# Kernel optimization log

Hardware: AMD Instinct MI355X
Metric: run time of the kernel (lower is better)

The kernel has to match this reference:

```python
import jax, jax.numpy as jnp
import numpy as np

D_MODEL = 1024
N_HEADS = 16
D_KEYS = D_MODEL // N_HEADS


def setup_inputs() -> dict:
    key = jax.random.key(0)
    ks = jax.random.split(key, 11)
    B, L, S = 2, 2048, 2048
    inp = {
        "queries": jax.random.normal(ks[0], (B, L, D_MODEL), dtype=jnp.float32),
        "keys": jax.random.normal(ks[1], (B, S, D_MODEL), dtype=jnp.float32),
        "values": jax.random.normal(ks[2], (B, S, D_MODEL), dtype=jnp.float32),
        # Linear params, scaled like torch default init (~U(-1/sqrt(D), 1/sqrt(D)))
        "Wq": jax.random.normal(ks[3], (D_MODEL, D_MODEL), dtype=jnp.float32) / np.sqrt(D_MODEL),
        "bq": jax.random.normal(ks[4], (D_MODEL,), dtype=jnp.float32) / np.sqrt(D_MODEL),
        "Wk": jax.random.normal(ks[5], (D_MODEL, D_MODEL), dtype=jnp.float32) / np.sqrt(D_MODEL),
        "bk": jax.random.normal(ks[6], (D_MODEL,), dtype=jnp.float32) / np.sqrt(D_MODEL),
        "Wv": jax.random.normal(ks[7], (D_MODEL, D_MODEL), dtype=jnp.float32) / np.sqrt(D_MODEL),
        "bv": jax.random.normal(ks[8], (D_MODEL,), dtype=jnp.float32) / np.sqrt(D_MODEL),
        "Wo": jax.random.normal(ks[9], (D_MODEL, D_MODEL), dtype=jnp.float32) / np.sqrt(D_MODEL),
        "bo": jax.random.normal(ks[10], (D_MODEL,), dtype=jnp.float32) / np.sqrt(D_MODEL),
    }
    return inp


def reference(queries, keys, values, Wq, bq, Wk, bk, Wv, bv, Wo, bo):
    B, L, _ = queries.shape
    S = keys.shape[1]
    H, E = N_HEADS, D_KEYS
    scale = E ** (-0.5)
    q = (queries @ Wq.T + bq).reshape(B, L, H, E)
    k = (keys @ Wk.T + bk).reshape(B, S, H, E)
    v = (values @ Wv.T + bv).reshape(B, S, H, E)
    scores = jnp.einsum('blhe,bshe->bhls', q, k)
    attn = jax.nn.softmax(scores * scale, axis=-1)  # dropout = identity in eval
    out = jnp.einsum('bhls,bshe->blhe', attn, v).reshape(B, L, H * E)
    return out @ Wo.T + bo
```

## Files before the change

kernel.cpp:

```cpp
#include <hip/hip_runtime.h>

typedef unsigned short u16;
typedef unsigned int u32;
typedef __attribute__((ext_vector_type(8))) short short8;
typedef __attribute__((ext_vector_type(4))) short s16x4;
typedef __attribute__((ext_vector_type(4))) float f32x4;
typedef __attribute__((ext_vector_type(16))) float f32x16;

#define DEVI __device__ __forceinline__

#define LSEQ 2048
#define DMODEL 1024
#define NH 16
#define EHD 64

#define QSCALE 0.18033688011112042f

#if __has_builtin(__builtin_amdgcn_exp2f)
#define EXP2(x) __builtin_amdgcn_exp2f(x)
#else
#define EXP2(x) exp2f(x)
#endif

DEVI u16 f2b(float f) {
    u32 u = __float_as_uint(f);
    return (u16)((u + 0x7FFFu + ((u >> 16) & 1u)) >> 16);
}

DEVI u32 cvtpk(float lo, float hi) {
    u32 r;
    asm("v_cvt_pk_bf16_f32 %0, %1, %2" : "=v"(r) : "v"(lo), "v"(hi));
    return r;
}

DEVI void swap32(u32& a, u32& b) {
    asm("v_permlane32_swap_b32 %0, %1" : "+v"(a), "+v"(b));
}

DEVI short8 mk8(u32 a0, u32 a1, u32 a2, u32 a3) {
    union { u32 u[4]; short8 s; } x;
    x.u[0] = a0; x.u[1] = a1; x.u[2] = a2; x.u[3] = a3;
    return x.s;
}

DEVI void async_cp16(const u16* g, u16* l) {
    __builtin_amdgcn_global_load_lds((const __attribute__((address_space(1))) u32*)g,
                                     (__attribute__((address_space(3))) u32*)l, 16, 0, 0);
}

DEVI short8 lds_swz(const u16* base, int row, int colb) {
    int off = (row << 7) + (colb ^ ((row & 7) << 4));
    return *(const short8*)((const char*)base + off);
}

__global__ __launch_bounds__(256) void cvt_all(const float* __restrict__ q,
                                               const float* __restrict__ k,
                                               const float* __restrict__ v,
                                               const float* __restrict__ wq,
                                               const float* __restrict__ wk,
                                               const float* __restrict__ wv,
                                               const float* __restrict__ wo,
                                               u16* __restrict__ dst) {
    const size_t NX8 = (size_t)2 * LSEQ * DMODEL / 8;
    const size_t NW8 = (size_t)DMODEL * DMODEL / 8;
    int bid = blockIdx.x;
    const float* src;
    size_t base;
    int rel;
    if (bid < 2048)      { src = q;  base = 0;             rel = bid; }
    else if (bid < 4096) { src = k;  base = NX8;           rel = bid - 2048; }
    else if (bid < 6144) { src = v;  base = 2 * NX8;       rel = bid - 4096; }
    else if (bid < 6656) { src = wq; base = 3 * NX8;             rel = bid - 6144; }
    else if (bid < 7168) { src = wk; base = 3 * NX8 + NW8;       rel = bid - 6656; }
    else if (bid < 7680) { src = wv; base = 3 * NX8 + 2 * NW8;   rel = bid - 7168; }
    else                 { src = wo; base = 3 * NX8 + 3 * NW8;   rel = bid - 7680; }
    size_t i = (size_t)rel * 256 + threadIdx.x;
    const float4* p = (const float4*)(src + i * 8);
    float4 a = p[0], c = p[1];
    short8 o;
    o[0] = (short)f2b(a.x); o[1] = (short)f2b(a.y);
    o[2] = (short)f2b(a.z); o[3] = (short)f2b(a.w);
    o[4] = (short)f2b(c.x); o[5] = (short)f2b(c.y);
    o[6] = (short)f2b(c.z); o[7] = (short)f2b(c.w);
    *(short8*)(dst + (base + i) * 8) = o;
}

__global__ __launch_bounds__(256) void gemm_qkv(const u16* __restrict__ X,
                                                const u16* __restrict__ W3,
                                                const float* __restrict__ bq,
                                                const float* __restrict__ bk,
                                                const float* __restrict__ bv,
                                                u16* __restrict__ Qp,
                                                u16* __restrict__ Kp,
                                                u16* __restrict__ Vt) {
    __shared__ __align__(16) u16 As[3][4096];
    __shared__ __align__(16) u16 Bs[3][4096];
    const int tid = threadIdx.x;
    const int lane = tid & 63, w = tid >> 6;
    const int lr = lane & 15, lk = lane >> 4;
    const int wr = w >> 1, wc = w & 1;
    const int bid = blockIdx.x;
    const int xcd = bid & 7, rr = bid >> 3;
    const int rb = (xcd * 4 + rr / 24) * 128;
    const int xtile = rr % 24;
    const int cb = xtile * 128;
    const int K = DMODEL;
    const int seg = xtile >> 3;
    const u16* A = X + (size_t)seg * ((size_t)2 * LSEQ * DMODEL);

    f32x4 acc[4][4] = {};

    const int arow = lane >> 2;
    const int acol = (lane & 3) * 8;

#define QKV_STAGE(bb, kk)                                                           \
    do {                                                                            \
        _Pragma("unroll") for (int c2 = 0; c2 < 2; ++c2) {                          \
            int c = w * 2 + c2;                                                     \
            async_cp16(A + (size_t)(rb + c * 16 + arow) * K + (kk) + acol,          \
                       &As[bb][c * 512]);                                           \
            async_cp16(W3 + (size_t)(cb + c * 16 + arow) * K + (kk) + acol,         \
                       &Bs[bb][c * 512]);                                           \
        }                                                                           \
    } while (0)

#define QKV_ITER(bc, bs, tt)                                                          \
    do {                                                                              \
        if ((tt) + 2 < 32) QKV_STAGE(bs, ((tt) + 2) * 32);                            \
        short8 af[4], bfr[4];                                                         \
        _Pragma("unroll") for (int m = 0; m < 4; m++)                                 \
            af[m] = *(const short8*)(&As[bc][(wr * 64 + m * 16 + lr) * 32 + lk * 8]); \
        _Pragma("unroll") for (int n = 0; n < 4; n++)                                 \
            bfr[n] = *(const short8*)(&Bs[bc][(wc * 64 + n * 16 + lr) * 32 + lk * 8]); \
        __builtin_amdgcn_s_setprio(1);                                                \
        _Pragma("unroll") for (int m = 0; m < 4; m++)                                 \
            _Pragma("unroll") for (int n = 0; n < 4; n++)                             \
                acc[m][n] =                                                           \
                    __builtin_amdgcn_mfma_f32_16x16x32_bf16(af[m], bfr[n], acc[m][n], 0, 0, 0); \
        __builtin_amdgcn_s_setprio(0);                                                \
        if ((tt) + 2 < 32) asm volatile("s_waitcnt vmcnt(4)" ::: "memory");           \
        else               asm volatile("s_waitcnt vmcnt(0)" ::: "memory");           \
        __builtin_amdgcn_s_barrier();                                                 \
    } while (0)

    QKV_STAGE(0, 0);
    QKV_STAGE(1, 32);
    asm volatile("s_waitcnt vmcnt(4)" ::: "memory");
    __builtin_amdgcn_s_barrier();

    for (int tb = 0; tb < 30; tb += 3) {
        QKV_ITER(0, 2, tb);
        QKV_ITER(1, 0, tb + 1);
        QKV_ITER(2, 1, tb + 2);
    }
    QKV_ITER(0, 2, 30);
    QKV_ITER(1, 0, 31);

    const float* bp = seg == 0 ? bq : (seg == 1 ? bk : bv);
    const float sc = seg == 0 ? QSCALE : 1.0f;

#pragma unroll
    for (int n = 0; n < 4; n++) {
        int col = cb + wc * 64 + n * 16 + lr;
        int c2 = col & 1023;
        float bvv = bp[c2];
#pragma unroll
        for (int m = 0; m < 4; m++) {
            int row0 = rb + wr * 64 + m * 16 + lk * 4;
            if (seg == 2) {
                s16x4 pk4;
#pragma unroll
                for (int r = 0; r < 4; r++) pk4[r] = (short)f2b(acc[m][n][r] + bvv);
                size_t idx = (((size_t)(row0 >> 11) * NH + (c2 >> 6)) * EHD + (c2 & 63)) * LSEQ +
                             (row0 & (LSEQ - 1));
                *(s16x4*)(Vt + idx) = pk4;
            } else {
                u16* dst = seg == 0 ? Qp : Kp;
#pragma unroll
                for (int r = 0; r < 4; r++)
                    dst[(size_t)(row0 + r) * DMODEL + c2] = f2b((acc[m][n][r] + bvv) * sc);
            }
        }
    }
}

__global__ __launch_bounds__(256) void gemm_out(const u16* __restrict__ A,
                                                const u16* __restrict__ B,
                                                const float* __restrict__ bias,
                                                float* __restrict__ C) {
    __shared__ __align__(16) u16 As[3][4096];
    __shared__ __align__(16) u16 Bs[3][2048];
    const int tid = threadIdx.x;
    const int lane = tid & 63, w = tid >> 6;
    const int lr = lane & 15, lk = lane >> 4;
    const int wr = w >> 1, wc = w & 1;
    const int bid = blockIdx.x;
    const int xcd = bid & 7, rr = bid >> 3;
    const int rb = (xcd * 4 + rr / 16) * 128;
    const int cb = (rr % 16) * 64;
    const int K = DMODEL, N = DMODEL;

    f32x4 acc[4][2] = {};

    const int arow = lane >> 2;
    const int acol = (lane & 3) * 8;

#define OUT_STAGE(bb, kk)                                                           \
    do {                                                                            \
        _Pragma("unroll") for (int c2 = 0; c2 < 2; ++c2) {                          \
            int c = w * 2 + c2;                                                     \
            async_cp16(A + (size_t)(rb + c * 16 + arow) * K + (kk) + acol,          \
                       &As[bb][c * 512]);                                           \
        }                                                                           \
        async_cp16(B + (size_t)(cb + w * 16 + arow) * K + (kk) + acol,              \
                   &Bs[bb][w * 512]);                                               \
    } while (0)

#define OUT_ITER(bc, bs, tt)                                                          \
    do {                                                                              \
        if ((tt) + 2 < 32) OUT_STAGE(bs, ((tt) + 2) * 32);                            \
        short8 af[4], bfr[2];                                                         \
        _Pragma("unroll") for (int m = 0; m < 4; m++)                                 \
            af[m] = *(const short8*)(&As[bc][(wr * 64 + m * 16 + lr) * 32 + lk * 8]); \
        _Pragma("unroll") for (int n = 0; n < 2; n++)                                 \
            bfr[n] = *(const short8*)(&Bs[bc][(wc * 32 + n * 16 + lr) * 32 + lk * 8]); \
        __builtin_amdgcn_s_setprio(1);                                                \
        _Pragma("unroll") for (int m = 0; m < 4; m++)                                 \
            _Pragma("unroll") for (int n = 0; n < 2; n++)                             \
                acc[m][n] =                                                           \
                    __builtin_amdgcn_mfma_f32_16x16x32_bf16(af[m], bfr[n], acc[m][n], 0, 0, 0); \
        __builtin_amdgcn_s_setprio(0);                                                \
        if ((tt) + 2 < 32) asm volatile("s_waitcnt vmcnt(3)" ::: "memory");           \
        else               asm volatile("s_waitcnt vmcnt(0)" ::: "memory");           \
        __builtin_amdgcn_s_barrier();                                                 \
    } while (0)

    OUT_STAGE(0, 0);
    OUT_STAGE(1, 32);
    asm volatile("s_waitcnt vmcnt(3)" ::: "memory");
    __builtin_amdgcn_s_barrier();

    for (int tb = 0; tb < 30; tb += 3) {
        OUT_ITER(0, 2, tb);
        OUT_ITER(1, 0, tb + 1);
        OUT_ITER(2, 1, tb + 2);
    }
    OUT_ITER(0, 2, 30);
    OUT_ITER(1, 0, 31);

#pragma unroll
    for (int n = 0; n < 2; n++) {
        int col = cb + wc * 32 + n * 16 + lr;
        float bv = bias[col];
#pragma unroll
        for (int m = 0; m < 4; m++) {
            int row0 = rb + wr * 64 + m * 16 + lk * 4;
#pragma unroll
            for (int r = 0; r < 4; r++)
                C[(size_t)(row0 + r) * N + col] = acc[m][n][r] + bv;
        }
    }
}

__global__ __launch_bounds__(256) void attn_kernel(const u16* __restrict__ Q,
                                                   const u16* __restrict__ Kp,
                                                   const u16* __restrict__ Vtb,
                                                   u16* __restrict__ Hid) {
    const int bid = blockIdx.x;
    const int j = bid >> 3;
    const int bh = (bid & 7) + 8 * (j >> 4);
    const int q0 = (j & 15) * 128;
    const int b = bh >> 4, h = bh & 15;
    const int tid = threadIdx.x, lane = tid & 63, w = tid >> 6;
    const int l31 = lane & 31, hi = lane >> 5;
    const int qb = q0 + w * 32;

    __shared__ __align__(16) u16 Ks[2][4096];
    __shared__ __align__(16) u16 Vs[2][4096];

    short8 qf[4];
#pragma unroll
    for (int eg = 0; eg < 4; eg++)
        qf[eg] = *(const short8*)(Q + (size_t)(b * LSEQ + qb + l31) * DMODEL + h * EHD +
                                  eg * 16 + hi * 8);

    const int colb = (((lane & 7) ^ (lane >> 3)) << 4);
    size_t kbase[2], vbase[2];
#pragma unroll
    for (int jj = 0; jj < 2; jj++) {
        int row = (jj * 4 + w) * 8 + (lane >> 3);
        kbase[jj] = (size_t)(b * LSEQ + row) * DMODEL + h * EHD + (colb >> 1);
        vbase[jj] = ((size_t)bh * EHD + row) * LSEQ + (colb >> 1);
    }

#define ATTN_STAGE(bb, s0v)                                                           \
    do {                                                                              \
        async_cp16(Kp + kbase[0] + (size_t)(s0v)*DMODEL, &Ks[bb][(0 * 4 + w) * 512]); \
        async_cp16(Kp + kbase[1] + (size_t)(s0v)*DMODEL, &Ks[bb][(1 * 4 + w) * 512]); \
        async_cp16(Vtb + vbase[0] + (s0v), &Vs[bb][(0 * 4 + w) * 512]);               \
        async_cp16(Vtb + vbase[1] + (s0v), &Vs[bb][(1 * 4 + w) * 512]);               \
    } while (0)

    f32x16 o0 = (f32x16)0.f, o1 = (f32x16)0.f, lsum = (f32x16)0.f;
    const u32 one2 = 0x3F803F80u;
    const short8 ones = mk8(one2, one2, one2, one2);

    ATTN_STAGE(0, 0);
    asm volatile("s_waitcnt vmcnt(0)" ::: "memory");
    __syncthreads();

    int cur = 0;
    for (int t = 0; t < LSEQ / 64; ++t) {
        if (t + 1 < LSEQ / 64) ATTN_STAGE(cur ^ 1, (t + 1) * 64);

        f32x16 s0 = (f32x16)0.f, s1 = (f32x16)0.f;
        __builtin_amdgcn_s_setprio(1);
#pragma unroll
        for (int eg = 0; eg < 4; eg++) {
            short8 kf0 = lds_swz(&Ks[cur][0], l31, eg * 32 + hi * 16);
            short8 kf1 = lds_swz(&Ks[cur][0], 32 + l31, eg * 32 + hi * 16);
            s0 = __builtin_amdgcn_mfma_f32_32x32x16_bf16(kf0, qf[eg], s0, 0, 0, 0);
            s1 = __builtin_amdgcn_mfma_f32_32x32x16_bf16(kf1, qf[eg], s1, 0, 0, 0);
        }
        __builtin_amdgcn_s_setprio(0);

#pragma unroll
        for (int r = 0; r < 16; r++) {
            s0[r] = EXP2(s0[r]);
            s1[r] = EXP2(s1[r]);
        }

        short8 paf[4];
#pragma unroll
        for (int kc = 0; kc < 4; kc++) {
            int ro = (kc & 1) * 8;
            u32 u0, u1, u2, u3;
            if (kc < 2) {
                u0 = cvtpk(s0[ro + 0], s0[ro + 1]); u1 = cvtpk(s0[ro + 2], s0[ro + 3]);
                u2 = cvtpk(s0[ro + 4], s0[ro + 5]); u3 = cvtpk(s0[ro + 6], s0[ro + 7]);
            } else {
                u0 = cvtpk(s1[ro + 0], s1[ro + 1]); u1 = cvtpk(s1[ro + 2], s1[ro + 3]);
                u2 = cvtpk(s1[ro + 4], s1[ro + 5]); u3 = cvtpk(s1[ro + 6], s1[ro + 7]);
            }
            swap32(u0, u2);
            swap32(u1, u3);
            paf[kc] = mk8(u0, u1, u2, u3);
        }

        __builtin_amdgcn_s_setprio(1);
#pragma unroll
        for (int kc = 0; kc < 4; kc++) {
            short8 vf0 = lds_swz(&Vs[cur][0], l31, kc * 32 + hi * 16);
            short8 vf1 = lds_swz(&Vs[cur][0], 32 + l31, kc * 32 + hi * 16);
            o0 = __builtin_amdgcn_mfma_f32_32x32x16_bf16(paf[kc], vf0, o0, 0, 0, 0);
            o1 = __builtin_amdgcn_mfma_f32_32x32x16_bf16(paf[kc], vf1, o1, 0, 0, 0);
            lsum = __builtin_amdgcn_mfma_f32_32x32x16_bf16(paf[kc], ones, lsum, 0, 0, 0);
        }
        __builtin_amdgcn_s_setprio(0);

        asm volatile("s_waitcnt vmcnt(0)" ::: "memory");
        __syncthreads();
        cur ^= 1;
    }

#pragma unroll
    for (int r = 0; r < 16; r++) {
        float li = 1.0f / lsum[r];
        int qrow = qb + (r & 3) + 8 * (r >> 2) + 4 * hi;
        size_t base = (size_t)(b * LSEQ + qrow) * DMODEL + h * EHD;
        Hid[base + l31] = f2b(o0[r] * li);
        Hid[base + 32 + l31] = f2b(o1[r] * li);
    }
}

extern "C" void kernel_launch(void* const* d_in, const int* in_sizes, int n_in,
                              void* d_out, int out_size, void* d_ws, size_t ws_size,
                              hipStream_t stream) {
    const float* queries = (const float*)d_in[0];
    const float* keys    = (const float*)d_in[1];
    const float* values  = (const float*)d_in[2];
    const float* Wq = (const float*)d_in[3];
    const float* bq = (const float*)d_in[4];
    const float* Wk = (const float*)d_in[5];
    const float* bk = (const float*)d_in[6];
    const float* Wv = (const float*)d_in[7];
    const float* bv = (const float*)d_in[8];
    const float* Wo = (const float*)d_in[9];
    const float* bo = (const float*)d_in[10];
    float* out = (float*)d_out;

    const size_t NX = (size_t)2 * LSEQ * DMODEL;
    const size_t NW = (size_t)DMODEL * DMODEL;

    u16* p = (u16*)d_ws;
    u16* Xq = p;  p += NX;
    u16* Xk = p;  p += NX;
    u16* Xv = p;  p += NX;
    u16* Wqb = p; p += NW;
    u16* Wkb = p; p += NW;
    u16* Wvb = p; p += NW;
    u16* Wob = p; p += NW;
    u16* Qp = p;  p += NX;
    u16* Kp = p;  p += NX;
    u16* Vt = p;  p += NX;
    u16* Hid = p; p += NX;
    (void)Xk; (void)Xv; (void)Wkb; (void)Wvb;

    cvt_all<<<8192, 256, 0, stream>>>(queries, keys, values, Wq, Wk, Wv, Wo, Xq);

    gemm_qkv<<<768, 256, 0, stream>>>(Xq, Wqb, bq, bk, bv, Qp, Kp, Vt);

    attn_kernel<<<512, 256, 0, stream>>>(Qp, Kp, Vt, Hid);

    gemm_out<<<512, 256, 0, stream>>>(Hid, Wob, bo, out);
}
```

Before: 136.7 us.

## Fuse fp32-to-bf16 activation conversion into QKV GEMM A-tile loads

Removes the separate conversion pass over the query/key/value activations. The QKV GEMM now reads fp32 activations directly into registers, converts them to bf16 and writes them into LDS. Only the weights are still pre-converted by a smaller kernel. This avoids writing and re-reading three bf16 activation buffers, but the A tile now goes through registers instead of async global-to-LDS copies, and each A tile is reloaded in fp32 by every column-tile block.

```diff
diff --git a/kernel.cpp b/kernel.cpp
--- a/kernel.cpp
+++ b/kernel.cpp
@@ -53,27 +53,15 @@
     return *(const short8*)((const char*)base + off);
 }
 
-__global__ __launch_bounds__(256) void cvt_all(const float* __restrict__ q,
-                                               const float* __restrict__ k,
-                                               const float* __restrict__ v,
-                                               const float* __restrict__ wq,
-                                               const float* __restrict__ wk,
-                                               const float* __restrict__ wv,
-                                               const float* __restrict__ wo,
-                                               u16* __restrict__ dst) {
-    const size_t NX8 = (size_t)2 * LSEQ * DMODEL / 8;
-    const size_t NW8 = (size_t)DMODEL * DMODEL / 8;
+__global__ __launch_bounds__(256) void cvt_w(const float* __restrict__ wq,
+                                             const float* __restrict__ wk,
+                                             const float* __restrict__ wv,
+                                             const float* __restrict__ wo,
+                                             u16* __restrict__ dst) {
     int bid = blockIdx.x;
-    const float* src;
-    size_t base;
-    int rel;
-    if (bid < 2048)      { src = q;  base = 0;             rel = bid; }
-    else if (bid < 4096) { src = k;  base = NX8;           rel = bid - 2048; }
-    else if (bid < 6144) { src = v;  base = 2 * NX8;       rel = bid - 4096; }
-    else if (bid < 6656) { src = wq; base = 3 * NX8;             rel = bid - 6144; }
-    else if (bid < 7168) { src = wk; base = 3 * NX8 + NW8;       rel = bid - 6656; }
-    else if (bid < 7680) { src = wv; base = 3 * NX8 + 2 * NW8;   rel = bid - 7168; }
-    else                 { src = wo; base = 3 * NX8 + 3 * NW8;   rel = bid - 7680; }
+    const float* src = bid < 512 ? wq : (bid < 1024 ? wk : (bid < 1536 ? wv : wo));
+    int rel = bid & 511;
+    size_t base = (size_t)(bid >> 9) * ((size_t)DMODEL * DMODEL);
     size_t i = (size_t)rel * 256 + threadIdx.x;
     const float4* p = (const float4*)(src + i * 8);
     float4 a = p[0], c = p[1];
@@ -82,10 +70,12 @@
     o[2] = (short)f2b(a.z); o[3] = (short)f2b(a.w);
     o[4] = (short)f2b(c.x); o[5] = (short)f2b(c.y);
     o[6] = (short)f2b(c.z); o[7] = (short)f2b(c.w);
-    *(short8*)(dst + (base + i) * 8) = o;
-}
-
-__global__ __launch_bounds__(256) void gemm_qkv(const u16* __restrict__ X,
+    *(short8*)(dst + base + i * 8) = o;
+}
+
+__global__ __launch_bounds__(256) void gemm_qkv(const float* __restrict__ Xq,
+                                                const float* __restrict__ Xk,
+                                                const float* __restrict__ Xv,
                                                 const u16* __restrict__ W3,
                                                 const float* __restrict__ bq,
                                                 const float* __restrict__ bk,
@@ -106,47 +96,88 @@
     const int cb = xtile * 128;
     const int K = DMODEL;
     const int seg = xtile >> 3;
-    const u16* A = X + (size_t)seg * ((size_t)2 * LSEQ * DMODEL);
+    const float* A = seg == 0 ? Xq : (seg == 1 ? Xk : Xv);
 
     f32x4 acc[4][4] = {};
 
     const int arow = lane >> 2;
     const int acol = (lane & 3) * 8;
-
-#define QKV_STAGE(bb, kk)                                                           \
-    do {                                                                            \
-        _Pragma("unroll") for (int c2 = 0; c2 < 2; ++c2) {                          \
-            int c = w * 2 + c2;                                                     \
-            async_cp16(A + (size_t)(rb + c * 16 + arow) * K + (kk) + acol,          \
-                       &As[bb][c * 512]);                                           \
-            async_cp16(W3 + (size_t)(cb + c * 16 + arow) * K + (kk) + acol,         \
-                       &Bs[bb][c * 512]);                                           \
-        }                                                                           \
+    const int sr = w * 8 + (lane >> 3);
+    const int sc = (lane & 7) * 4;
+
+#define QKV_CVTW(bs, jrow, avv)                                                        \
+    do {                                                                               \
+        u32* wp = (u32*)&As[bs][((jrow) + sr) * 32 + sc];                              \
+        wp[0] = cvtpk((avv).x, (avv).y);                                               \
+        wp[1] = cvtpk((avv).z, (avv).w);                                               \
     } while (0)
 
-#define QKV_ITER(bc, bs, tt)                                                          \
-    do {                                                                              \
-        if ((tt) + 2 < 32) QKV_STAGE(bs, ((tt) + 2) * 32);                            \
-        short8 af[4], bfr[4];                                                         \
-        _Pragma("unroll") for (int m = 0; m < 4; m++)                                 \
-            af[m] = *(const short8*)(&As[bc][(wr * 64 + m * 16 + lr) * 32 + lk * 8]); \
-        _Pragma("unroll") for (int n = 0; n < 4; n++)                                 \
+#define QKV_ITER(bc, bs, tt)                                                           \
+    do {                                                                               \
+        float4 av0, av1, av2, av3;                                                     \
+        const bool st = (tt) + 2 < 32;                                                 \
+        if (st) {                                                                      \
+            const float* ap = A + (size_t)(rb + sr) * K + ((tt) + 2) * 32 + sc;        \
+            av0 = *(const float4*)(ap);                                                \
+            av1 = *(const float4*)(ap + 32 * K);                                       \
+            av2 = *(const float4*)(ap + 64 * K);                                       \
+            av3 = *(const float4*)(ap + 96 * K);                                       \
+            async_cp16(W3 + (size_t)(cb + (w * 2 + 0) * 16 + arow) * K + ((tt) + 2) * 32 + acol, \
+                       &Bs[bs][(w * 2 + 0) * 512]);                                    \
+            async_cp16(W3 + (size_t)(cb + (w * 2 + 1) * 16 + arow) * K + ((tt) + 2) * 32 + acol, \
+                       &Bs[bs][(w * 2 + 1) * 512]);                                    \
+        }                                                                              \
+        short8 af[4], bfr[4];                                                          \
+        _Pragma("unroll") for (int m = 0; m < 4; m++)                                  \
+            af[m] = *(const short8*)(&As[bc][(wr * 64 + m * 16 + lr) * 32 + lk * 8]);  \
+        _Pragma("unroll") for (int n = 0; n < 4; n++)                                  \
             bfr[n] = *(const short8*)(&Bs[bc][(wc * 64 + n * 16 + lr) * 32 + lk * 8]); \
-        __builtin_amdgcn_s_setprio(1);                                                \
-        _Pragma("unroll") for (int m = 0; m < 4; m++)                                 \
-            _Pragma("unroll") for (int n = 0; n < 4; n++)                             \
-                acc[m][n] =                                                           \
+        __builtin_amdgcn_s_setprio(1);                                                 \
+        _Pragma("unroll") for (int m = 0; m < 4; m++)                                  \
+            _Pragma("unroll") for (int n = 0; n < 4; n++)                              \
+                acc[m][n] =                                                            \
                     __builtin_amdgcn_mfma_f32_16x16x32_bf16(af[m], bfr[n], acc[m][n], 0, 0, 0); \
-        __builtin_amdgcn_s_setprio(0);                                                \
-        if ((tt) + 2 < 32) asm volatile("s_waitcnt vmcnt(4)" ::: "memory");           \
-        else               asm volatile("s_waitcnt vmcnt(0)" ::: "memory");           \
-        __builtin_amdgcn_s_barrier();                                                 \
+        __builtin_amdgcn_s_setprio(0);                                                 \
+        __builtin_amdgcn_sched_barrier(0);                                             \
+        if (st) {                                                                      \
+            QKV_CVTW(bs, 0, av0);                                                      \
+            QKV_CVTW(bs, 32, av1);                                                     \
+            QKV_CVTW(bs, 64, av2);                                                     \
+            QKV_CVTW(bs, 96, av3);                                                     \
+            asm volatile("s_waitcnt vmcnt(2)" ::: "memory");                           \
+        } else {                                                                       \
+            asm volatile("s_waitcnt vmcnt(0)" ::: "memory");                           \
+        }                                                                              \
+        asm volatile("s_waitcnt lgkmcnt(0)" ::: "memory");                             \
+        __builtin_amdgcn_s_barrier();                                                  \
     } while (0)
 
-    QKV_STAGE(0, 0);
-    QKV_STAGE(1, 32);
-    asm volatile("s_waitcnt vmcnt(4)" ::: "memory");
-    __builtin_amdgcn_s_barrier();
+    {
+        const float* ap = A + (size_t)(rb + sr) * K + sc;
+        float4 a00 = *(const float4*)(ap);
+        float4 a01 = *(const float4*)(ap + 32 * K);
+        float4 a02 = *(const float4*)(ap + 64 * K);
+        float4 a03 = *(const float4*)(ap + 96 * K);
+        float4 a10 = *(const float4*)(ap + 32);
+        float4 a11 = *(const float4*)(ap + 32 * K + 32);
+        float4 a12 = *(const float4*)(ap + 64 * K + 32);
+        float4 a13 = *(const float4*)(ap + 96 * K + 32);
+        async_cp16(W3 + (size_t)(cb + (w * 2 + 0) * 16 + arow) * K + acol, &Bs[0][(w * 2 + 0) * 512]);
+        async_cp16(W3 + (size_t)(cb + (w * 2 + 1) * 16 + arow) * K + acol, &Bs[0][(w * 2 + 1) * 512]);
+        async_cp16(W3 + (size_t)(cb + (w * 2 + 0) * 16 + arow) * K + 32 + acol, &Bs[1][(w * 2 + 0) * 512]);
+        async_cp16(W3 + (size_t)(cb + (w * 2 + 1) * 16 + arow) * K + 32 + acol, &Bs[1][(w * 2 + 1) * 512]);
+        QKV_CVTW(0, 0, a00);
+        QKV_CVTW(0, 32, a01);
+        QKV_CVTW(0, 64, a02);
+        QKV_CVTW(0, 96, a03);
+        QKV_CVTW(1, 0, a10);
+        QKV_CVTW(1, 32, a11);
+        QKV_CVTW(1, 64, a12);
+        QKV_CVTW(1, 96, a13);
+        asm volatile("s_waitcnt vmcnt(2)" ::: "memory");
+        asm volatile("s_waitcnt lgkmcnt(0)" ::: "memory");
+        __builtin_amdgcn_s_barrier();
+    }
 
     for (int tb = 0; tb < 30; tb += 3) {
         QKV_ITER(0, 2, tb);
@@ -157,7 +188,7 @@
     QKV_ITER(1, 0, 31);
 
     const float* bp = seg == 0 ? bq : (seg == 1 ? bk : bv);
-    const float sc = seg == 0 ? QSCALE : 1.0f;
+    const float sc2 = seg == 0 ? QSCALE : 1.0f;
 
 #pragma unroll
     for (int n = 0; n < 4; n++) {
@@ -178,7 +209,7 @@
                 u16* dst = seg == 0 ? Qp : Kp;
 #pragma unroll
                 for (int r = 0; r < 4; r++)
-                    dst[(size_t)(row0 + r) * DMODEL + c2] = f2b((acc[m][n][r] + bvv) * sc);
+                    dst[(size_t)(row0 + r) * DMODEL + c2] = f2b((acc[m][n][r] + bvv) * sc2);
             }
         }
     }
@@ -393,9 +424,6 @@
     const size_t NW = (size_t)DMODEL * DMODEL;
 
     u16* p = (u16*)d_ws;
-    u16* Xq = p;  p += NX;
-    u16* Xk = p;  p += NX;
-    u16* Xv = p;  p += NX;
     u16* Wqb = p; p += NW;
     u16* Wkb = p; p += NW;
     u16* Wvb = p; p += NW;
@@ -404,11 +432,11 @@
     u16* Kp = p;  p += NX;
     u16* Vt = p;  p += NX;
     u16* Hid = p; p += NX;
-    (void)Xk; (void)Xv; (void)Wkb; (void)Wvb;
-
-    cvt_all<<<8192, 256, 0, stream>>>(queries, keys, values, Wq, Wk, Wv, Wo, Xq);
-
-    gemm_qkv<<<768, 256, 0, stream>>>(Xq, Wqb, bq, bk, bv, Qp, Kp, Vt);
+    (void)Wkb; (void)Wvb;
+
+    cvt_w<<<2048, 256, 0, stream>>>(Wq, Wk, Wv, Wo, Wqb);
+
+    gemm_qkv<<<768, 256, 0, stream>>>(queries, keys, values, Wqb, bq, bk, bv, Qp, Kp, Vt);
 
     attn_kernel<<<512, 256, 0, stream>>>(Qp, Kp, Vt, Hid);
 
```

Measured after the change: 140.0 us. +2.4%, slower.

## Enlarge attention blocks to 512 threads with 128-key tiles

Applied to the files above, without the earlier changes.

The attention kernel now runs 256 blocks of 512 threads, each covering 256 queries instead of 128, so each K/V tile loaded into shared memory is reused by twice as many waves. The key loop advances 128 keys per step, processed as two 64-key halves, which halves the number of barriers and waits per key. The cost is twice the shared memory per block and fewer, larger blocks across the CUs, which may reduce occupancy or leave CUs unevenly loaded.

```diff
diff --git a/kernel.cpp b/kernel.cpp
--- a/kernel.cpp
+++ b/kernel.cpp
@@ -262,21 +262,21 @@
     }
 }
 
-__global__ __launch_bounds__(256) void attn_kernel(const u16* __restrict__ Q,
+__global__ __launch_bounds__(512) void attn_kernel(const u16* __restrict__ Q,
                                                    const u16* __restrict__ Kp,
                                                    const u16* __restrict__ Vtb,
                                                    u16* __restrict__ Hid) {
     const int bid = blockIdx.x;
     const int j = bid >> 3;
-    const int bh = (bid & 7) + 8 * (j >> 4);
-    const int q0 = (j & 15) * 128;
+    const int bh = (bid & 7) + 8 * (j >> 3);
+    const int q0 = (j & 7) * 256;
     const int b = bh >> 4, h = bh & 15;
     const int tid = threadIdx.x, lane = tid & 63, w = tid >> 6;
     const int l31 = lane & 31, hi = lane >> 5;
     const int qb = q0 + w * 32;
 
-    __shared__ __align__(16) u16 Ks[2][4096];
-    __shared__ __align__(16) u16 Vs[2][4096];
+    __shared__ __align__(16) u16 Ks[2][8192];
+    __shared__ __align__(16) u16 Vs[2][2][4096];
 
     short8 qf[4];
 #pragma unroll
@@ -284,21 +284,22 @@
         qf[eg] = *(const short8*)(Q + (size_t)(b * LSEQ + qb + l31) * DMODEL + h * EHD +
                                   eg * 16 + hi * 8);
 
-    const int colb = (((lane & 7) ^ (lane >> 3)) << 4);
+    const int trow = tid >> 3;
+    const int slot = tid & 7;
+    const int swz8 = ((slot ^ (trow & 7)) * 8);
     size_t kbase[2], vbase[2];
 #pragma unroll
     for (int jj = 0; jj < 2; jj++) {
-        int row = (jj * 4 + w) * 8 + (lane >> 3);
-        kbase[jj] = (size_t)(b * LSEQ + row) * DMODEL + h * EHD + (colb >> 1);
-        vbase[jj] = ((size_t)bh * EHD + row) * LSEQ + (colb >> 1);
+        kbase[jj] = (size_t)(b * LSEQ + jj * 64 + trow) * DMODEL + h * EHD + swz8;
+        vbase[jj] = ((size_t)bh * EHD + trow) * LSEQ + jj * 64 + swz8;
     }
 
 #define ATTN_STAGE(bb, s0v)                                                           \
     do {                                                                              \
-        async_cp16(Kp + kbase[0] + (size_t)(s0v)*DMODEL, &Ks[bb][(0 * 4 + w) * 512]); \
-        async_cp16(Kp + kbase[1] + (size_t)(s0v)*DMODEL, &Ks[bb][(1 * 4 + w) * 512]); \
-        async_cp16(Vtb + vbase[0] + (s0v), &Vs[bb][(0 * 4 + w) * 512]);               \
-        async_cp16(Vtb + vbase[1] + (s0v), &Vs[bb][(1 * 4 + w) * 512]);               \
+        async_cp16(Kp + kbase[0] + (size_t)(s0v)*DMODEL, &Ks[bb][w * 512]);           \
+        async_cp16(Kp + kbase[1] + (size_t)(s0v)*DMODEL, &Ks[bb][4096 + w * 512]);    \
+        async_cp16(Vtb + vbase[0] + (s0v), &Vs[bb][0][w * 512]);                      \
+        async_cp16(Vtb + vbase[1] + (s0v), &Vs[bb][1][w * 512]);                      \
     } while (0)
 
     f32x16 o0 = (f32x16)0.f, o1 = (f32x16)0.f, lsum = (f32x16)0.f;
@@ -310,53 +311,56 @@
     __syncthreads();
 
     int cur = 0;
-    for (int t = 0; t < LSEQ / 64; ++t) {
-        if (t + 1 < LSEQ / 64) ATTN_STAGE(cur ^ 1, (t + 1) * 64);
-
-        f32x16 s0 = (f32x16)0.f, s1 = (f32x16)0.f;
-        __builtin_amdgcn_s_setprio(1);
-#pragma unroll
-        for (int eg = 0; eg < 4; eg++) {
-            short8 kf0 = lds_swz(&Ks[cur][0], l31, eg * 32 + hi * 16);
-            short8 kf1 = lds_swz(&Ks[cur][0], 32 + l31, eg * 32 + hi * 16);
-            s0 = __builtin_amdgcn_mfma_f32_32x32x16_bf16(kf0, qf[eg], s0, 0, 0, 0);
-            s1 = __builtin_amdgcn_mfma_f32_32x32x16_bf16(kf1, qf[eg], s1, 0, 0, 0);
+    for (int t = 0; t < LSEQ / 128; ++t) {
+        if (t + 1 < LSEQ / 128) ATTN_STAGE(cur ^ 1, (t + 1) * 128);
+
+#pragma unroll
+        for (int hf = 0; hf < 2; hf++) {
+            f32x16 s0 = (f32x16)0.f, s1 = (f32x16)0.f;
+            __builtin_amdgcn_s_setprio(1);
+#pragma unroll
+            for (int eg = 0; eg < 4; eg++) {
+                short8 kf0 = lds_swz(&Ks[cur][0], hf * 64 + l31, eg * 32 + hi * 16);
+                short8 kf1 = lds_swz(&Ks[cur][0], hf * 64 + 32 + l31, eg * 32 + hi * 16);
+                s0 = __builtin_amdgcn_mfma_f32_32x32x16_bf16(kf0, qf[eg], s0, 0, 0, 0);
+                s1 = __builtin_amdgcn_mfma_f32_32x32x16_bf16(kf1, qf[eg], s1, 0, 0, 0);
+            }
+            __builtin_amdgcn_s_setprio(0);
+
+#pragma unroll
+            for (int r = 0; r < 16; r++) {
+                s0[r] = EXP2(s0[r]);
+                s1[r] = EXP2(s1[r]);
+            }
+
+            short8 paf[4];
+#pragma unroll
+            for (int kc = 0; kc < 4; kc++) {
+                int ro = (kc & 1) * 8;
+                u32 u0, u1, u2, u3;
+                if (kc < 2) {
+                    u0 = cvtpk(s0[ro + 0], s0[ro + 1]); u1 = cvtpk(s0[ro + 2], s0[ro + 3]);
+                    u2 = cvtpk(s0[ro + 4], s0[ro + 5]); u3 = cvtpk(s0[ro + 6], s0[ro + 7]);
+                } else {
+                    u0 = cvtpk(s1[ro + 0], s1[ro + 1]); u1 = cvtpk(s1[ro + 2], s1[ro + 3]);
+                    u2 = cvtpk(s1[ro + 4], s1[ro + 5]); u3 = cvtpk(s1[ro + 6], s1[ro + 7]);
+                }
+                swap32(u0, u2);
+                swap32(u1, u3);
+                paf[kc] = mk8(u0, u1, u2, u3);
+            }
+
+            __builtin_amdgcn_s_setprio(1);
+#pragma unroll
+            for (int kc = 0; kc < 4; kc++) {
+                short8 vf0 = lds_swz(&Vs[cur][hf][0], l31, kc * 32 + hi * 16);
+                short8 vf1 = lds_swz(&Vs[cur][hf][0], 32 + l31, kc * 32 + hi * 16);
+                o0 = __builtin_amdgcn_mfma_f32_32x32x16_bf16(paf[kc], vf0, o0, 0, 0, 0);
+                o1 = __builtin_amdgcn_mfma_f32_32x32x16_bf16(paf[kc], vf1, o1, 0, 0, 0);
+                lsum = __builtin_amdgcn_mfma_f32_32x32x16_bf16(paf[kc], ones, lsum, 0, 0, 0);
+            }
+            __builtin_amdgcn_s_setprio(0);
         }
-        __builtin_amdgcn_s_setprio(0);
-
-#pragma unroll
-        for (int r = 0; r < 16; r++) {
-            s0[r] = EXP2(s0[r]);
-            s1[r] = EXP2(s1[r]);
-        }
-
-        short8 paf[4];
-#pragma unroll
-        for (int kc = 0; kc < 4; kc++) {
-            int ro = (kc & 1) * 8;
-            u32 u0, u1, u2, u3;
-            if (kc < 2) {
-                u0 = cvtpk(s0[ro + 0], s0[ro + 1]); u1 = cvtpk(s0[ro + 2], s0[ro + 3]);
-                u2 = cvtpk(s0[ro + 4], s0[ro + 5]); u3 = cvtpk(s0[ro + 6], s0[ro + 7]);
-            } else {
-                u0 = cvtpk(s1[ro + 0], s1[ro + 1]); u1 = cvtpk(s1[ro + 2], s1[ro + 3]);
-                u2 = cvtpk(s1[ro + 4], s1[ro + 5]); u3 = cvtpk(s1[ro + 6], s1[ro + 7]);
-            }
-            swap32(u0, u2);
-            swap32(u1, u3);
-            paf[kc] = mk8(u0, u1, u2, u3);
-        }
-
-        __builtin_amdgcn_s_setprio(1);
-#pragma unroll
-        for (int kc = 0; kc < 4; kc++) {
-            short8 vf0 = lds_swz(&Vs[cur][0], l31, kc * 32 + hi * 16);
-            short8 vf1 = lds_swz(&Vs[cur][0], 32 + l31, kc * 32 + hi * 16);
-            o0 = __builtin_amdgcn_mfma_f32_32x32x16_bf16(paf[kc], vf0, o0, 0, 0, 0);
-            o1 = __builtin_amdgcn_mfma_f32_32x32x16_bf16(paf[kc], vf1, o1, 0, 0, 0);
-            lsum = __builtin_amdgcn_mfma_f32_32x32x16_bf16(paf[kc], ones, lsum, 0, 0, 0);
-        }
-        __builtin_amdgcn_s_setprio(0);
 
         asm volatile("s_waitcnt vmcnt(0)" ::: "memory");
         __syncthreads();
@@ -410,7 +414,7 @@
 
     gemm_qkv<<<768, 256, 0, stream>>>(Xq, Wqb, bq, bk, bv, Qp, Kp, Vt);
 
-    attn_kernel<<<512, 256, 0, stream>>>(Qp, Kp, Vt, Hid);
+    attn_kernel<<<256, 512, 0, stream>>>(Qp, Kp, Vt, Hid);
 
     gemm_out<<<512, 256, 0, stream>>>(Hid, Wob, bo, out);
 }
```

Result: faster. 130.7 us (-4.4%).
